# Performance work log

Measured on AMD Instinct MI355X. Metric: run time of the kernel, lower is better.

## Reference

```python
import jax, jax.numpy as jnp
import numpy as np

N_NODES = 50000
N_EDGES = 800000
N_GRAPHS = 500
IN_CH = 128
HID = 128
OUT_CH = 10
N_LAYERS = 3


def setup_inputs() -> dict:
    key = jax.random.key(0)
    ks = jax.random.split(key, 12)
    s_in = 1.0 / np.sqrt(IN_CH)
    s_h = 1.0 / np.sqrt(HID)
    inp = {
        "x": jax.random.normal(ks[0], (N_NODES, IN_CH), jnp.float32),
        "conv_w1": jax.random.normal(ks[1], (N_LAYERS, HID, HID), jnp.float32) * s_in,
        "conv_b1": jax.random.normal(ks[2], (N_LAYERS, HID), jnp.float32) * s_in,
        "conv_w2": jax.random.normal(ks[3], (N_LAYERS, HID, HID), jnp.float32) * s_h,
        "conv_b2": jax.random.normal(ks[4], (N_LAYERS, HID), jnp.float32) * s_h,
        "mlp_w1": jax.random.normal(ks[5], (HID, HID), jnp.float32) * s_h,
        "mlp_b1": jax.random.normal(ks[6], (HID,), jnp.float32) * s_h,
        "mlp_w2": jax.random.normal(ks[7], (HID, OUT_CH), jnp.float32) * s_h,
        "mlp_b2": jax.random.normal(ks[8], (OUT_CH,), jnp.float32) * s_h,
        "edge_index": jax.random.randint(ks[9], (2, N_EDGES), 0, N_NODES, jnp.int64),
        "batch": jnp.sort(jax.random.randint(ks[10], (N_NODES,), 0, N_GRAPHS, jnp.int64)),
    }
    return inp


def reference(x, conv_w1, conv_b1, conv_w2, conv_b2,
              mlp_w1, mlp_b1, mlp_w2, mlp_b2, edge_index, batch):
    src, dst = edge_index[0], edge_index[1]
    n = x.shape[0]
    for l in range(conv_w1.shape[0]):
        # GINConv, eps=0: h_i = mlp(x_i + sum_{j in N(i)} x_j)
        agg = jax.ops.segment_sum(x[src], dst, num_segments=n)  # [N, d]
        h = x + agg
        h = jnp.maximum(h @ conv_w1[l] + conv_b1[l], 0.0) @ conv_w2[l] + conv_b2[l]
        x = jnp.maximum(h, 0.0)  # outer F.relu(conv(...))
    # global_add_pool over graph ids
    g = jax.ops.segment_sum(x, batch, num_segments=N_GRAPHS)  # [G, HID]
    # final MLP (dropout is identity in eval)
    h = jnp.maximum(g @ mlp_w1 + mlp_b1, 0.0)
    return h @ mlp_w2 + mlp_b2
```

## Files before the change

kernel.cpp:

```cpp
#include <hip/hip_runtime.h>

#define NODES   50000
#define EDGES   800000
#define GRAPHS  500
#define HID     128
#define OUTC    10
#define NLAYERS 3
#define ELLCAP  64

typedef __bf16 bf16x8 __attribute__((ext_vector_type(8)));
typedef float  f32x4  __attribute__((ext_vector_type(4)));

__device__ __forceinline__ unsigned short f2bf(float f){
    unsigned u = __float_as_uint(f);
    u = (u + 0x7fffu + ((u >> 16) & 1u)) >> 16;
    return (unsigned short)u;
}
__device__ __forceinline__ float bf2f(unsigned short h){
    return __uint_as_float(((unsigned)h) << 16);
}

#define FGRPS  8
#define GSZ    (NODES / FGRPS)
#define GCAP   131072
#define FILLB  ((EDGES + 255) / 256)
#define PREPB  ((6 * HID * HID + 255) / 256)
#define CONVB  ((NODES * 64 + 255) / 256)
#define FPB2   98

__global__ __launch_bounds__(256) void setup_kernel(
    const int* __restrict__ src, const int* __restrict__ dst,
    unsigned* __restrict__ ep, int* __restrict__ gcnt,
    const float* __restrict__ w1, const float* __restrict__ w2,
    unsigned short* __restrict__ wt,
    const float* __restrict__ x, unsigned* __restrict__ xb)
{
    const int b = blockIdx.x;
    if (b < FILLB) {
        __shared__ int lcnt[FGRPS], lbase[FGRPS];
        const int tid = threadIdx.x;
        int e = b * 256 + tid;
        if (tid < FGRPS) lcnt[tid] = 0;
        __syncthreads();
        int d = 0, s = 0, grp = 0, lpos = 0;
        bool ok = e < EDGES;
        if (ok) {
            d = dst[e]; s = src[e];
            grp = d / GSZ;
            lpos = atomicAdd(&lcnt[grp], 1);
        }
        __syncthreads();
        if (tid < FGRPS) lbase[tid] = atomicAdd(&gcnt[tid], lcnt[tid]);
        __syncthreads();
        if (ok) {
            int pos = lbase[grp] + lpos;
            if (pos < GCAP)
                ep[(size_t)grp * GCAP + pos] =
                    ((unsigned)(d - grp * GSZ) << 16) | (unsigned)s;
        }
    } else if (b < FILLB + PREPB) {
        int idx = (b - FILLB) * 256 + threadIdx.x;
        if (idx < 6 * HID * HID) {
            int m = idx >> 14;
            int n = (idx >> 7) & 127;
            int k = idx & 127;
            const float* w = (m < 3) ? (w1 + (size_t)m * HID * HID)
                                     : (w2 + (size_t)(m - 3) * HID * HID);
            wt[idx] = f2bf(w[(size_t)k * HID + n]);
        }
    } else {
        int i = (b - FILLB - PREPB) * 256 + threadIdx.x;
        if (i < NODES * 64) {
            float2 v = reinterpret_cast<const float2*>(x)[i];
            xb[i] = ((unsigned)f2bf(v.y) << 16) | f2bf(v.x);
        }
    }
}

__global__ __launch_bounds__(256) void fill2_kernel(
    const unsigned* __restrict__ ep, const int* __restrict__ gcnt,
    int* __restrict__ deg, unsigned short* __restrict__ ell)
{
    const int grp = blockIdx.x & 7;
    const int bi  = blockIdx.x >> 3;
    const int n0  = grp * GSZ;
    const int cnt = min(gcnt[grp], GCAP);
    const unsigned* p = ep + (size_t)grp * GCAP;
    for (int e = bi * 256 + threadIdx.x; e < cnt; e += FPB2 * 256) {
        unsigned r = p[e];
        int d = n0 + (int)(r >> 16);
        int s = (int)(r & 0xffffu);
        int pos = atomicAdd(&deg[d], 1);
        if (pos < ELLCAP) ell[(size_t)pos * NODES + d] = (unsigned short)s;
    }
}

__global__ __launch_bounds__(512) void layer_kernel(
    const unsigned short* __restrict__ X,
    const int* __restrict__ deg, const unsigned short* __restrict__ ell,
    const unsigned short* __restrict__ Wt1, const float* __restrict__ bias1,
    const unsigned short* __restrict__ Wt2, const float* __restrict__ bias2,
    unsigned short* __restrict__ C)
{
    __shared__ unsigned short As[32][136];
    __shared__ unsigned short idx_s[ELLCAP][32];
    __shared__ int deg_s[32];
    const int tid  = threadIdx.x;
    const int w    = tid >> 6;
    const int lane = tid & 63;
    const int q    = lane >> 4;
    const int lr   = lane & 15;
    const int row0 = blockIdx.x * 32;

    const uint4* xr = reinterpret_cast<const uint4*>(X);

    if (tid < 32) {
        int n = row0 + tid;
        if (n >= NODES) n = NODES - 1;
        deg_s[tid] = min(deg[n], ELLCAP);
    }
    __syncthreads();

    int maxd = 0;
    #pragma unroll
    for (int i = 0; i < 32; ++i) maxd = max(maxd, deg_s[i]);

    {
        const int sl0 = tid >> 5;
        const int nn  = tid & 31;
        int gn = row0 + nn;
        if (gn >= NODES) gn = NODES - 1;
        for (int s = sl0; s < maxd; s += 16)
            idx_s[s][nn] = ell[(size_t)s * NODES + gn];
    }
    __syncthreads();

    for (int i = 0; i < 4; ++i) {
        const int row = w * 4 + i;
        int n = row0 + row;
        if (n >= NODES) n = NODES - 1;

        float acc[8];
        #pragma unroll
        for (int k = 0; k < 8; ++k) acc[k] = 0.f;

        const int dg = deg_s[row];
        for (int e0 = 0; e0 < dg; e0 += 16) {
            uint4 v[4];
            unsigned m[4];
            #pragma unroll
            for (int j = 0; j < 4; ++j) {
                int e = e0 + 4 * j + q;
                bool ok = e < dg;
                m[j] = ok ? 0xffffffffu : 0u;
                int ec = ok ? e : 0;
                int s = idx_s[ec][row];
                v[j] = xr[(size_t)s * 16 + lr];
            }
            #pragma unroll
            for (int j = 0; j < 4; ++j) {
                const unsigned uu[4] = {v[j].x, v[j].y, v[j].z, v[j].w};
                #pragma unroll
                for (int k2 = 0; k2 < 4; ++k2) {
                    unsigned uv = uu[k2] & m[j];
                    acc[2 * k2]     += __uint_as_float(uv << 16);
                    acc[2 * k2 + 1] += __uint_as_float(uv & 0xffff0000u);
                }
            }
        }

        #pragma unroll
        for (int k = 0; k < 8; ++k) {
            acc[k] += __shfl_xor(acc[k], 16, 64);
            acc[k] += __shfl_xor(acc[k], 32, 64);
        }

        if (q == 0) {
            uint4 self = xr[(size_t)n * 16 + lr];
            const unsigned su[4] = {self.x, self.y, self.z, self.w};
            uint4 o;
            unsigned* ou = &o.x;
            #pragma unroll
            for (int j = 0; j < 4; ++j) {
                float c0 = acc[2 * j]     + __uint_as_float(su[j] << 16);
                float c1 = acc[2 * j + 1] + __uint_as_float(su[j] & 0xffff0000u);
                ou[j] = ((unsigned)f2bf(c1) << 16) | f2bf(c0);
            }
            *reinterpret_cast<uint4*>(&As[row][lr * 8]) = o;
        }
    }
    __syncthreads();

    const int rg = w >> 2;
    const int cq = w & 3;
    const int ar = rg * 16 + lr;

    bf16x8 af[4];
    f32x4 acc[2];

    #pragma unroll
    for (int s = 0; s < 4; ++s)
        af[s] = *reinterpret_cast<const bf16x8*>(&As[ar][s * 32 + q * 8]);
    __syncthreads();

    #pragma unroll
    for (int nt = 0; nt < 2; ++nt) acc[nt] = (f32x4){0.f, 0.f, 0.f, 0.f};
    {
        #pragma unroll
        for (int nt = 0; nt < 2; ++nt) {
            const unsigned short* wn = Wt1 + (size_t)(cq * 32 + nt * 16 + lr) * HID + q * 8;
            #pragma unroll
            for (int s = 0; s < 4; ++s) {
                bf16x8 b = *reinterpret_cast<const bf16x8*>(wn + s * 32);
                acc[nt] = __builtin_amdgcn_mfma_f32_16x16x32_bf16(b, af[s], acc[nt], 0, 0, 0);
            }
        }
    }

    {
        const float4* b4p = reinterpret_cast<const float4*>(bias1);
        #pragma unroll
        for (int nt = 0; nt < 2; ++nt) {
            int col = cq * 32 + nt * 16 + q * 4;
            float4 b4 = b4p[col >> 2];
            ushort4 o;
            o.x = f2bf(fmaxf(acc[nt][0] + b4.x, 0.f));
            o.y = f2bf(fmaxf(acc[nt][1] + b4.y, 0.f));
            o.z = f2bf(fmaxf(acc[nt][2] + b4.z, 0.f));
            o.w = f2bf(fmaxf(acc[nt][3] + b4.w, 0.f));
            *reinterpret_cast<ushort4*>(&As[ar][col]) = o;
        }
    }
    __syncthreads();

    #pragma unroll
    for (int s = 0; s < 4; ++s)
        af[s] = *reinterpret_cast<const bf16x8*>(&As[ar][s * 32 + q * 8]);
    #pragma unroll
    for (int nt = 0; nt < 2; ++nt) acc[nt] = (f32x4){0.f, 0.f, 0.f, 0.f};
    {
        #pragma unroll
        for (int nt = 0; nt < 2; ++nt) {
            const unsigned short* wn = Wt2 + (size_t)(cq * 32 + nt * 16 + lr) * HID + q * 8;
            #pragma unroll
            for (int s = 0; s < 4; ++s) {
                bf16x8 b = *reinterpret_cast<const bf16x8*>(wn + s * 32);
                acc[nt] = __builtin_amdgcn_mfma_f32_16x16x32_bf16(b, af[s], acc[nt], 0, 0, 0);
            }
        }
    }

    const int row = row0 + ar;
    if (row < NODES) {
        const float4* b4p = reinterpret_cast<const float4*>(bias2);
        #pragma unroll
        for (int nt = 0; nt < 2; ++nt) {
            int col = cq * 32 + nt * 16 + q * 4;
            float4 b4 = b4p[col >> 2];
            ushort4 o;
            o.x = f2bf(fmaxf(acc[nt][0] + b4.x, 0.f));
            o.y = f2bf(fmaxf(acc[nt][1] + b4.y, 0.f));
            o.z = f2bf(fmaxf(acc[nt][2] + b4.z, 0.f));
            o.w = f2bf(fmaxf(acc[nt][3] + b4.w, 0.f));
            *reinterpret_cast<ushort4*>(C + (size_t)row * HID + col) = o;
        }
    }
}

__device__ __forceinline__ int lbound(const int* __restrict__ a, int v)
{
    int lo = 0, hi = NODES;
    while (lo < hi) {
        int m = (lo + hi) >> 1;
        if (a[m] < v) lo = m + 1; else hi = m;
    }
    return lo;
}

__global__ __launch_bounds__(256) void pool_mlp_kernel(
    const unsigned short* __restrict__ x,
    const int* __restrict__ batch,
    const float* __restrict__ mw1, const float* __restrict__ mb1,
    const float* __restrict__ mw2, const float* __restrict__ mb2,
    float* __restrict__ out)
{
    const int gid = blockIdx.x;
    const int beg = lbound(batch, gid);
    const int end = lbound(batch, gid + 1);

    const int c    = threadIdx.x & 127;
    const int half = threadIdx.x >> 7;

    float acc = 0.f;
    for (int r = beg + half; r < end; r += 2)
        acc += bf2f(x[(size_t)r * HID + c]);

    __shared__ float lds[256];
    __shared__ float gl[128];
    __shared__ float gh[128];
    lds[threadIdx.x] = acc;
    __syncthreads();
    if (threadIdx.x < 128)
        gl[threadIdx.x] = lds[threadIdx.x] + lds[threadIdx.x + 128];
    __syncthreads();

    if (threadIdx.x < 128) {
        float a = mb1[threadIdx.x];
        #pragma unroll 8
        for (int k = 0; k < 128; ++k)
            a += gl[k] * mw1[(size_t)k * HID + threadIdx.x];
        gh[threadIdx.x] = fmaxf(a, 0.f);
    }
    __syncthreads();

    if (threadIdx.x < OUTC) {
        float a = mb2[threadIdx.x];
        #pragma unroll 8
        for (int k = 0; k < 128; ++k)
            a += gh[k] * mw2[(size_t)k * OUTC + threadIdx.x];
        out[(size_t)gid * OUTC + threadIdx.x] = a;
    }
}

extern "C" void kernel_launch(void* const* d_in, const int* in_sizes, int n_in,
                              void* d_out, int out_size, void* d_ws, size_t ws_size,
                              hipStream_t stream)
{
    const float* x    = (const float*)d_in[0];
    const float* w1   = (const float*)d_in[1];
    const float* b1   = (const float*)d_in[2];
    const float* w2   = (const float*)d_in[3];
    const float* b2   = (const float*)d_in[4];
    const float* mw1  = (const float*)d_in[5];
    const float* mb1  = (const float*)d_in[6];
    const float* mw2  = (const float*)d_in[7];
    const float* mb2  = (const float*)d_in[8];
    const int*   ei   = (const int*)d_in[9];
    const int*   batch= (const int*)d_in[10];
    float* out = (float*)d_out;

    char* p = (char*)d_ws;
    unsigned short* buf0 = (unsigned short*)p;  p += (size_t)NODES * HID * 2;
    unsigned short* buf1 = (unsigned short*)p;  p += (size_t)NODES * HID * 2;
    unsigned short* ell  = (unsigned short*)p;  p += (size_t)NODES * ELLCAP * 2;
    unsigned short* wt   = (unsigned short*)p;  p += (size_t)6 * HID * HID * 2;
    unsigned* ep  = (unsigned*)p;               p += (size_t)FGRPS * GCAP * 4;
    int*   deg    = (int*)p;                    p += (size_t)NODES * 4;
    int*   gcnt   = (int*)p;                    p += FGRPS * 4;

    const int* src = ei;
    const int* dst = ei + EDGES;

    const int layerBlocks = (NODES + 31) / 32;
    const int setupBlocks = FILLB + PREPB + CONVB;

    hipMemsetAsync(deg, 0, ((size_t)NODES + FGRPS) * sizeof(int), stream);
    setup_kernel<<<setupBlocks, 256, 0, stream>>>(
        src, dst, ep, gcnt, w1, w2, wt, x, (unsigned*)buf0);
    fill2_kernel<<<FGRPS * FPB2, 256, 0, stream>>>(ep, gcnt, deg, ell);

    unsigned short* bin  = buf0;
    unsigned short* bout = buf1;
    for (int l = 0; l < NLAYERS; ++l) {
        layer_kernel<<<layerBlocks, 512, 0, stream>>>(
            bin, deg, ell,
            wt + (size_t)l * HID * HID,       b1 + (size_t)l * HID,
            wt + (size_t)(l + 3) * HID * HID, b2 + (size_t)l * HID,
            bout);
        unsigned short* t = bin; bin = bout; bout = t;
    }

    pool_mlp_kernel<<<GRAPHS, 256, 0, stream>>>(bin, batch, mw1, mb1, mw2, mb2, out);
}
```

Baseline: 275.8 us.

## Build ELL adjacency in setup by per-group dst filtering, drop bucket pass

Replaces the two-pass edge bucketing (an intermediate per-group buffer plus a second fill kernel) with a single pass inside the setup kernel. Each of the 8 destination groups scans all edges and inserts only those whose destination falls in its range, directly into the ELL structure via atomic degree counters. This removes one kernel launch and the intermediate write and read of the edge buffer. In exchange, the dst array is read 8 times and the atomics land on scattered nodes instead of group-local ones.

```diff
diff --git a/kernel.cpp b/kernel.cpp
--- a/kernel.cpp
+++ b/kernel.cpp
@@ -21,42 +21,32 @@
 }
 
 #define FGRPS  8
+#define FPB    392
+#define FILLB  (FGRPS * FPB)
 #define GSZ    (NODES / FGRPS)
-#define GCAP   131072
-#define FILLB  ((EDGES + 255) / 256)
 #define PREPB  ((6 * HID * HID + 255) / 256)
 #define CONVB  ((NODES * 64 + 255) / 256)
-#define FPB2   98
 
 __global__ __launch_bounds__(256) void setup_kernel(
     const int* __restrict__ src, const int* __restrict__ dst,
-    unsigned* __restrict__ ep, int* __restrict__ gcnt,
+    int* __restrict__ deg, unsigned short* __restrict__ ell,
     const float* __restrict__ w1, const float* __restrict__ w2,
     unsigned short* __restrict__ wt,
     const float* __restrict__ x, unsigned* __restrict__ xb)
 {
     const int b = blockIdx.x;
     if (b < FILLB) {
-        __shared__ int lcnt[FGRPS], lbase[FGRPS];
-        const int tid = threadIdx.x;
-        int e = b * 256 + tid;
-        if (tid < FGRPS) lcnt[tid] = 0;
-        __syncthreads();
-        int d = 0, s = 0, grp = 0, lpos = 0;
-        bool ok = e < EDGES;
-        if (ok) {
-            d = dst[e]; s = src[e];
-            grp = d / GSZ;
-            lpos = atomicAdd(&lcnt[grp], 1);
-        }
-        __syncthreads();
-        if (tid < FGRPS) lbase[tid] = atomicAdd(&gcnt[tid], lcnt[tid]);
-        __syncthreads();
-        if (ok) {
-            int pos = lbase[grp] + lpos;
-            if (pos < GCAP)
-                ep[(size_t)grp * GCAP + pos] =
-                    ((unsigned)(d - grp * GSZ) << 16) | (unsigned)s;
+        const int grp = b & 7;
+        const int bi  = b >> 3;
+        const int lo  = grp * GSZ;
+        const int hi  = lo + GSZ;
+        for (int e = bi * 256 + threadIdx.x; e < EDGES; e += FPB * 256) {
+            int d = dst[e];
+            if (d >= lo && d < hi) {
+                int pos = atomicAdd(&deg[d], 1);
+                if (pos < ELLCAP)
+                    ell[(size_t)pos * NODES + d] = (unsigned short)src[e];
+            }
         }
     } else if (b < FILLB + PREPB) {
         int idx = (b - FILLB) * 256 + threadIdx.x;
@@ -74,24 +64,6 @@
             float2 v = reinterpret_cast<const float2*>(x)[i];
             xb[i] = ((unsigned)f2bf(v.y) << 16) | f2bf(v.x);
         }
-    }
-}
-
-__global__ __launch_bounds__(256) void fill2_kernel(
-    const unsigned* __restrict__ ep, const int* __restrict__ gcnt,
-    int* __restrict__ deg, unsigned short* __restrict__ ell)
-{
-    const int grp = blockIdx.x & 7;
-    const int bi  = blockIdx.x >> 3;
-    const int n0  = grp * GSZ;
-    const int cnt = min(gcnt[grp], GCAP);
-    const unsigned* p = ep + (size_t)grp * GCAP;
-    for (int e = bi * 256 + threadIdx.x; e < cnt; e += FPB2 * 256) {
-        unsigned r = p[e];
-        int d = n0 + (int)(r >> 16);
-        int s = (int)(r & 0xffffu);
-        int pos = atomicAdd(&deg[d], 1);
-        if (pos < ELLCAP) ell[(size_t)pos * NODES + d] = (unsigned short)s;
     }
 }
 
@@ -344,9 +316,7 @@
     unsigned short* buf1 = (unsigned short*)p;  p += (size_t)NODES * HID * 2;
     unsigned short* ell  = (unsigned short*)p;  p += (size_t)NODES * ELLCAP * 2;
     unsigned short* wt   = (unsigned short*)p;  p += (size_t)6 * HID * HID * 2;
-    unsigned* ep  = (unsigned*)p;               p += (size_t)FGRPS * GCAP * 4;
     int*   deg    = (int*)p;                    p += (size_t)NODES * 4;
-    int*   gcnt   = (int*)p;                    p += FGRPS * 4;
 
     const int* src = ei;
     const int* dst = ei + EDGES;
@@ -354,10 +324,9 @@
     const int layerBlocks = (NODES + 31) / 32;
     const int setupBlocks = FILLB + PREPB + CONVB;
 
-    hipMemsetAsync(deg, 0, ((size_t)NODES + FGRPS) * sizeof(int), stream);
+    hipMemsetAsync(deg, 0, (size_t)NODES * sizeof(int), stream);
     setup_kernel<<<setupBlocks, 256, 0, stream>>>(
-        src, dst, ep, gcnt, w1, w2, wt, x, (unsigned*)buf0);
-    fill2_kernel<<<FGRPS * FPB2, 256, 0, stream>>>(ep, gcnt, deg, ell);
+        src, dst, deg, ell, w1, w2, wt, x, (unsigned*)buf0);
 
     unsigned short* bin  = buf0;
     unsigned short* bout = buf1;
```

Result: faster. 236.4 us (-14.3%).
